# Optimization experiments

Measured on AMD Instinct MI355X. Metric: run time of the kernel, lower is better.

Reference implementation:

```python
import jax, jax.numpy as jnp
import numpy as np

TAU = 0.5  # temperature from init_kwargs


def _semi_loss(h1, h2):
    # GRACE-style InfoNCE: -log( e^{sim(i,i')/tau} / (sum_refl + sum_between - e^{sim(i,i)/tau}) )
    n1 = h1 / jnp.linalg.norm(h1, axis=1, keepdims=True)
    n2 = h2 / jnp.linalg.norm(h2, axis=1, keepdims=True)
    refl = jnp.exp((n1 @ n1.T) / TAU)   # [N, N]
    betw = jnp.exp((n1 @ n2.T) / TAU)   # [N, N]
    denom = refl.sum(axis=1) + betw.sum(axis=1) - jnp.diagonal(refl)
    return -jnp.log(jnp.diagonal(betw) / denom)


def _contrast(h1, h2):
    # forward_v1 with batch_size=0 (batched path is mathematically identical)
    return (0.5 * (_semi_loss(h1, h2) + _semi_loss(h2, h1))).mean()


def _proj(z, Wa, ba, Wb, bb):
    # fc_b(elu(fc_a(z))); torch Linear: y = x @ W.T + b
    return jax.nn.elu(z @ Wa.T + ba) @ Wb.T + bb


def setup_inputs() -> dict:
    key = jax.random.key(0)
    ks = jax.random.split(key, 11)
    N, A, B = 8192, 32, 32
    D = A * B
    s = 1.0 / np.sqrt(D)
    inp = {
        'ta': jax.random.normal(ks[0], (N, A, B), dtype=jnp.float32),
        'tb': jax.random.normal(ks[1], (N, A, B), dtype=jnp.float32),
        'W1': jax.random.uniform(ks[2], (D, D), jnp.float32, -s, s),
        'b1': jax.random.uniform(ks[3], (D,), jnp.float32, -s, s),
        'W2': jax.random.uniform(ks[4], (D, D), jnp.float32, -s, s),
        'b2': jax.random.uniform(ks[5], (D,), jnp.float32, -s, s),
        'W3': jax.random.uniform(ks[6], (D, D), jnp.float32, -s, s),
        'b3': jax.random.uniform(ks[7], (D,), jnp.float32, -s, s),
        'W4': jax.random.uniform(ks[8], (D, D), jnp.float32, -s, s),
        'b4': jax.random.uniform(ks[9], (D,), jnp.float32, -s, s),
        'w_r1': jnp.array([0.5], dtype=jnp.float32),
    }
    return inp


def reference(ta, tb, W1, b1, W2, b2, W3, b3, W4, b4, w_r1):
    N = ta.shape[0]
    # row view: [N, A*B]
    z1 = ta.reshape(N, -1)
    z2 = tb.reshape(N, -1)
    loss_row = _contrast(_proj(z1, W1, b1, W2, b2), _proj(z2, W1, b1, W2, b2))
    # column view: permute(0,2,1) then flatten -> [N, B*A]
    z1c = jnp.transpose(ta, (0, 2, 1)).reshape(N, -1)
    z2c = jnp.transpose(tb, (0, 2, 1)).reshape(N, -1)
    loss_col = _contrast(_proj(z1c, W3, b3, W4, b4), _proj(z2c, W3, b3, W4, b4))
    w_row = jnp.clip(w_r1[0], 0.0, 1.0)
    return w_row * loss_row + (1.0 - w_row) * loss_col
```

## Files before the change

kernel.cpp:

```cpp
#include <hip/hip_runtime.h>
#include <stdint.h>


typedef unsigned short u16;
typedef __attribute__((ext_vector_type(8))) __bf16 bf16x8;
typedef __attribute__((ext_vector_type(4))) float f32x4;

#define NS 8192
#define DD 1024

__device__ __forceinline__ float bf2f(u16 u) {
    union { uint32_t i; float f; } v; v.i = ((uint32_t)u) << 16; return v.f;
}
__device__ __forceinline__ u16 f2bf(float f) {
    union { float f; uint32_t i; } v; v.f = f;
    return (u16)((v.i + 0x7FFFu + ((v.i >> 16) & 1u)) >> 16);
}

__device__ __forceinline__ void gload16(const u16* g, u16* l) {
    __builtin_amdgcn_global_load_lds(
        (__attribute__((address_space(1))) void*)(uintptr_t)(g),
        (__attribute__((address_space(3))) void*)(uintptr_t)(l), 16, 0, 0);
}


__global__ __launch_bounds__(256) void conv_f2bf(const float* __restrict__ src,
                                                 u16* __restrict__ dst) {
    int i = (blockIdx.x * 256 + threadIdx.x) * 4;
    float4 v = *(const float4*)(src + i);
    ushort4 o;
    o.x = f2bf(v.x); o.y = f2bf(v.y); o.z = f2bf(v.z); o.w = f2bf(v.w);
    *(ushort4*)(dst + i) = o;
}

__global__ __launch_bounds__(256) void conv_cat(const float* __restrict__ a,
                                                const float* __restrict__ b,
                                                u16* __restrict__ Z) {
    size_t i = (size_t)(blockIdx.x * 256 + threadIdx.x) * 4;
    const size_t half = (size_t)NS * DD;
    const float* s = (i < half) ? (a + i) : (b + (i - half));
    float4 v = *(const float4*)s;
    ushort4 o;
    o.x = f2bf(v.x); o.y = f2bf(v.y); o.z = f2bf(v.z); o.w = f2bf(v.w);
    *(ushort4*)(Z + i) = o;
}

__global__ __launch_bounds__(256) void conv_col(const float* __restrict__ a,
                                                const float* __restrict__ b,
                                                u16* __restrict__ Z) {
    size_t i = (size_t)(blockIdx.x * 256 + threadIdx.x) * 4;
    const size_t half = (size_t)NS * DD;
    const float* src; size_t o;
    if (i < half) { src = a; o = i; } else { src = b; o = i - half; }
    size_t row = o >> 10;
    int j = (int)(o & 1023);
    int aI = j & 31, bI = j >> 5;
    const float* rp = src + (row << 10);
    ushort4 ov;
    ov.x = f2bf(rp[aI * 32 + bI]);
    ov.y = f2bf(rp[(aI + 1) * 32 + bI]);
    ov.z = f2bf(rp[(aI + 2) * 32 + bI]);
    ov.w = f2bf(rp[(aI + 3) * 32 + bI]);
    *(ushort4*)(Z + i) = ov;
}

template <int MODE>
__global__ __launch_bounds__(256) void gemm_bt(const u16* A, const u16* B,
                                               const float* __restrict__ bias,
                                               u16* __restrict__ out) {
    __shared__ alignas(16) u16 As[128 * 32];
    __shared__ alignas(16) u16 Bs[128 * 32];
    const int tid = threadIdx.x;

    const int tm = blockIdx.y, tn = blockIdx.x;
    const size_t tileM = (size_t)tm * 128;
    const size_t tileN = (size_t)tn * 128;

    const u16* gA0 = A + (tileM + (tid >> 2)) * DD + (tid & 3) * 8;
    const u16* gA1 = gA0 + (size_t)64 * DD;
    const u16* gB0 = B + (tileN + (tid >> 2)) * DD + (tid & 3) * 8;
    const u16* gB1 = gB0 + (size_t)64 * DD;
    u16* lA0 = &As[tid * 8]; u16* lA1 = lA0 + 2048;
    u16* lB0 = &Bs[tid * 8]; u16* lB1 = lB0 + 2048;

    const int lane = tid & 63;
    const int wv = tid >> 6;
    const int wr = (wv >> 1) << 6;
    const int wc = (wv & 1) << 6;
    const int lr = lane & 15;
    const int lh = lane >> 4;

    const u16* aBase = &As[(wr + lr) * 32 + lh * 8];
    const u16* bBase = &Bs[(wc + lr) * 32 + lh * 8];

    f32x4 acc[4][4];
#pragma unroll
    for (int i = 0; i < 4; i++)
#pragma unroll
        for (int j = 0; j < 4; j++) acc[i][j] = (f32x4)0.0f;

    for (int k0 = 0; k0 < DD; k0 += 32) {
        gload16(gA0 + k0, lA0);
        gload16(gA1 + k0, lA1);
        gload16(gB0 + k0, lB0);
        gload16(gB1 + k0, lB1);
        __syncthreads();
        bf16x8 af[4], bfr[4];
#pragma unroll
        for (int rt = 0; rt < 4; rt++) af[rt] = *(const bf16x8*)(aBase + rt * 512);
#pragma unroll
        for (int ct = 0; ct < 4; ct++) bfr[ct] = *(const bf16x8*)(bBase + ct * 512);
#pragma unroll
        for (int rt = 0; rt < 4; rt++)
#pragma unroll
            for (int ct = 0; ct < 4; ct++)
                acc[rt][ct] = __builtin_amdgcn_mfma_f32_16x16x32_bf16(
                    af[rt], bfr[ct], acc[rt][ct], 0, 0, 0);
        __syncthreads();
    }

    float bcol[4];
#pragma unroll
    for (int ct = 0; ct < 4; ct++) bcol[ct] = bias[tileN + wc + ct * 16 + lr];
#pragma unroll
    for (int rt = 0; rt < 4; rt++) {
#pragma unroll
        for (int r = 0; r < 4; r++) {
            size_t row = tileM + wr + rt * 16 + lh * 4 + r;
            u16* orow = out + row * DD + tileN + wc + lr;
#pragma unroll
            for (int ct = 0; ct < 4; ct++) {
                float v = acc[rt][ct][r] + bcol[ct];
                if (MODE == 0) v = v > 0.0f ? v : expm1f(v);
                orow[ct * 16] = f2bf(v);
            }
        }
    }
}

__global__ __launch_bounds__(512) void gram256(const u16* __restrict__ H,
                                               float* __restrict__ S) {
    __shared__ alignas(16) u16 LA[4][256 * 32];
    __shared__ alignas(16) u16 LB[4][256 * 32];
    const int tid = threadIdx.x;

    int x = blockIdx.x, y = blockIdx.y;
    int tm, tn;
    if (y + x < 64) { tm = y;      tn = y + x; }
    else            { tm = 63 - y; tn = x - 1; }

    const size_t rowA = (size_t)tm * 256;
    const size_t rowB = (size_t)tn * 256;

    const int r_lo = tid >> 2;
    const int s_st = tid & 3;
    const int csw  = (s_st ^ (r_lo & 3)) * 8;
    const u16* gA0 = H + (rowA + r_lo) * DD + csw;
    const u16* gA1 = H + (rowA + 128 + r_lo) * DD + csw;
    const u16* gB0 = H + (rowB + r_lo) * DD + csw;
    const u16* gB1 = H + (rowB + 128 + r_lo) * DD + csw;
    const int ldst = tid * 8;

    const int lane = tid & 63;
    const int wv = tid >> 6;
    const int wr = (wv >> 2) * 128;
    const int wc = (wv & 3) * 64;
    const int lr = lane & 15;
    const int lh = lane >> 4;
    const int sw = lh ^ (lr & 3);
    const int aoff = (wr + lr) * 32 + sw * 8;
    const int boff = (wc + lr) * 32 + sw * 8;

    f32x4 acc[8][4];
#pragma unroll
    for (int i = 0; i < 8; ++i)
#pragma unroll
        for (int j = 0; j < 4; ++j) acc[i][j] = (f32x4)0.0f;

#pragma unroll
    for (int t = 0; t < 3; ++t) {
        const int k0 = t * 32;
        gload16(gA0 + k0, &LA[t][0] + ldst);
        gload16(gA1 + k0, &LA[t][4096] + ldst);
        gload16(gB0 + k0, &LB[t][0] + ldst);
        gload16(gB1 + k0, &LB[t][4096] + ldst);
    }
    asm volatile("s_waitcnt vmcnt(8)" ::: "memory");
    __builtin_amdgcn_s_barrier();

    for (int t = 0; t < 32; ++t) {
        const int buf = t & 3;
        const u16* la = &LA[buf][0];
        const u16* lb = &LB[buf][0];
        const int nbuf = (t + 3) & 3;
        const int k0n = (t + 3) * 32;
        bf16x8 aF[4], bF[4];

#pragma unroll
        for (int i = 0; i < 4; ++i) aF[i] = *(const bf16x8*)(la + aoff + i * 512);
#pragma unroll
        for (int i = 0; i < 4; ++i) bF[i] = *(const bf16x8*)(lb + boff + i * 512);
        if (t < 29) {
            gload16(gA0 + k0n, &LA[nbuf][0] + ldst);
            gload16(gA1 + k0n, &LA[nbuf][4096] + ldst);
        }
        asm volatile("" ::: "memory");
        __builtin_amdgcn_s_barrier();
        asm volatile("s_waitcnt lgkmcnt(0)" ::: "memory");
        __builtin_amdgcn_sched_barrier(0);
        __builtin_amdgcn_s_setprio(1);
#pragma unroll
        for (int mi = 0; mi < 4; ++mi)
#pragma unroll
            for (int ni = 0; ni < 4; ++ni)
                acc[mi][ni] = __builtin_amdgcn_mfma_f32_16x16x32_bf16(
                    aF[mi], bF[ni], acc[mi][ni], 0, 0, 0);
        __builtin_amdgcn_s_setprio(0);
        __builtin_amdgcn_s_barrier();

#pragma unroll
        for (int i = 0; i < 4; ++i) aF[i] = *(const bf16x8*)(la + aoff + 2048 + i * 512);
        if (t < 29) {
            gload16(gB0 + k0n, &LB[nbuf][0] + ldst);
            gload16(gB1 + k0n, &LB[nbuf][4096] + ldst);
        }
        if (t < 29)       asm volatile("s_waitcnt vmcnt(8)" ::: "memory");
        else if (t == 29) asm volatile("s_waitcnt vmcnt(4)" ::: "memory");
        else if (t == 30) asm volatile("s_waitcnt vmcnt(0)" ::: "memory");
        __builtin_amdgcn_s_barrier();
        asm volatile("s_waitcnt lgkmcnt(0)" ::: "memory");
        __builtin_amdgcn_sched_barrier(0);
        __builtin_amdgcn_s_setprio(1);
#pragma unroll
        for (int mi = 0; mi < 4; ++mi)
#pragma unroll
            for (int ni = 0; ni < 4; ++ni)
                acc[4 + mi][ni] = __builtin_amdgcn_mfma_f32_16x16x32_bf16(
                    aF[mi], bF[ni], acc[4 + mi][ni], 0, 0, 0);
        __builtin_amdgcn_s_setprio(0);
        __builtin_amdgcn_s_barrier();
    }

    const bool offdiag = (tm != tn);
    float colsum[4] = {0.f, 0.f, 0.f, 0.f};
#pragma unroll
    for (int q = 0; q < 8; ++q) {
#pragma unroll
        for (int r = 0; r < 4; ++r) {
            float rs = 0.0f;
#pragma unroll
            for (int ni = 0; ni < 4; ++ni) {
                float e = __expf(2.0f * acc[q][ni][r]);
                rs += e;
                colsum[ni] += e;
            }
            rs += __shfl_xor(rs, 1);
            rs += __shfl_xor(rs, 2);
            rs += __shfl_xor(rs, 4);
            rs += __shfl_xor(rs, 8);
            if (lr == 0) {
                size_t row = rowA + wr + q * 16 + lh * 4 + r;
                atomicAdd(&S[row], rs);
            }
        }
    }
    if (offdiag) {
#pragma unroll
        for (int ni = 0; ni < 4; ++ni) {
            float cs = colsum[ni];
            cs += __shfl_xor(cs, 16);
            cs += __shfl_xor(cs, 32);
            if (lh == 0) {
                size_t col = rowB + wc + ni * 16 + lr;
                atomicAdd(&S[col], cs);
            }
        }
    }
}

__global__ __launch_bounds__(256) void normalize_kernel(u16* M) {
    __shared__ float red[4];
    const int tid = threadIdx.x;
    u16* row = M + ((size_t)blockIdx.x << 10);
    ushort4 v = ((const ushort4*)row)[tid];
    float x0 = bf2f(v.x), x1 = bf2f(v.y), x2 = bf2f(v.z), x3 = bf2f(v.w);
    float s = x0 * x0 + x1 * x1 + x2 * x2 + x3 * x3;
#pragma unroll
    for (int m = 1; m < 64; m <<= 1) s += __shfl_xor(s, m);
    if ((tid & 63) == 0) red[tid >> 6] = s;
    __syncthreads();
    float inv = rsqrtf(red[0] + red[1] + red[2] + red[3]);
    ushort4 o;
    o.x = f2bf(x0 * inv); o.y = f2bf(x1 * inv);
    o.z = f2bf(x2 * inv); o.w = f2bf(x3 * inv);
    ((ushort4*)row)[tid] = o;
}

__global__ __launch_bounds__(256) void diag_kernel(const u16* M, float* g12) {
    __shared__ float red[4];
    const int tid = threadIdx.x;
    const u16* r1 = M + ((size_t)blockIdx.x << 10);
    const u16* r2 = r1 + ((size_t)NS << 10);
    ushort4 a = ((const ushort4*)r1)[tid];
    ushort4 b = ((const ushort4*)r2)[tid];
    float s = bf2f(a.x) * bf2f(b.x) + bf2f(a.y) * bf2f(b.y) +
              bf2f(a.z) * bf2f(b.z) + bf2f(a.w) * bf2f(b.w);
#pragma unroll
    for (int m = 1; m < 64; m <<= 1) s += __shfl_xor(s, m);
    if ((tid & 63) == 0) red[tid >> 6] = s;
    __syncthreads();
    if (tid == 0) g12[blockIdx.x] = red[0] + red[1] + red[2] + red[3];
}

__global__ __launch_bounds__(256) void final_kernel(const float* Sr, const float* Sc,
                                                    const float* gr, const float* gc,
                                                    const float* w_r1, float* out) {
    __shared__ float red[16];
    const float E2 = 7.389056098930650f;
    float a = 0.f, b = 0.f, c = 0.f, d = 0.f;
    for (int i = threadIdx.x; i < 2 * NS; i += 256) {
        a += logf(Sr[i] - E2);
        b += logf(Sc[i] - E2);
    }
    for (int i = threadIdx.x; i < NS; i += 256) {
        c += gr[i];
        d += gc[i];
    }
#pragma unroll
    for (int m = 1; m < 64; m <<= 1) {
        a += __shfl_xor(a, m); b += __shfl_xor(b, m);
        c += __shfl_xor(c, m); d += __shfl_xor(d, m);
    }
    int w = threadIdx.x >> 6;
    if ((threadIdx.x & 63) == 0) {
        red[w] = a; red[4 + w] = b; red[8 + w] = c; red[12 + w] = d;
    }
    __syncthreads();
    if (threadIdx.x == 0) {
        a = red[0] + red[1] + red[2] + red[3];
        b = red[4] + red[5] + red[6] + red[7];
        c = red[8] + red[9] + red[10] + red[11];
        d = red[12] + red[13] + red[14] + red[15];
        float lr = a / (2.0f * NS) - 2.0f * c / NS;
        float lc = b / (2.0f * NS) - 2.0f * d / NS;
        float w0 = w_r1[0];
        w0 = fminf(fmaxf(w0, 0.0f), 1.0f);
        out[0] = w0 * lr + (1.0f - w0) * lc;
    }
}

extern "C" void kernel_launch(void* const* d_in, const int* in_sizes, int n_in,
                              void* d_out, int out_size, void* d_ws, size_t ws_size,
                              hipStream_t stream) {
    const float* ta = (const float*)d_in[0];
    const float* tb = (const float*)d_in[1];
    const float* W1 = (const float*)d_in[2];
    const float* b1 = (const float*)d_in[3];
    const float* W2 = (const float*)d_in[4];
    const float* b2 = (const float*)d_in[5];
    const float* W3 = (const float*)d_in[6];
    const float* b3 = (const float*)d_in[7];
    const float* W4 = (const float*)d_in[8];
    const float* b4 = (const float*)d_in[9];
    const float* wr = (const float*)d_in[10];
    float* out = (float*)d_out;

    char* p = (char*)d_ws;
    const size_t MAT = (size_t)2 * NS * DD * sizeof(u16);
    u16* Z = (u16*)p;  p += MAT;
    u16* T = (u16*)p;  p += MAT;
    u16* H = (u16*)p;  p += MAT;
    u16* Wb = (u16*)p; p += (size_t)4 * DD * DD * sizeof(u16);
    float* Sr = (float*)p;  p += 2 * NS * sizeof(float);
    float* Sc = (float*)p;  p += 2 * NS * sizeof(float);
    float* gr = (float*)p;  p += NS * sizeof(float);
    float* gc = (float*)p;  p += NS * sizeof(float);

    u16* Wb1 = Wb;
    u16* Wb2 = Wb + (size_t)DD * DD;
    u16* Wb3 = Wb + (size_t)2 * DD * DD;
    u16* Wb4 = Wb + (size_t)3 * DD * DD;

    conv_f2bf<<<1024, 256, 0, stream>>>(W1, Wb1);
    conv_f2bf<<<1024, 256, 0, stream>>>(W2, Wb2);
    conv_f2bf<<<1024, 256, 0, stream>>>(W3, Wb3);
    conv_f2bf<<<1024, 256, 0, stream>>>(W4, Wb4);
    hipMemsetAsync(Sr, 0, 4 * NS * sizeof(float), stream);

    conv_cat<<<16384, 256, 0, stream>>>(ta, tb, Z);
    gemm_bt<0><<<dim3(8, 128), 256, 0, stream>>>(Z, Wb1, b1, T);
    gemm_bt<1><<<dim3(8, 128), 256, 0, stream>>>(T, Wb2, b2, H);
    normalize_kernel<<<16384, 256, 0, stream>>>(H);
    diag_kernel<<<8192, 256, 0, stream>>>(H, gr);
    gram256<<<dim3(65, 32), 512, 0, stream>>>(H, Sr);

    conv_col<<<16384, 256, 0, stream>>>(ta, tb, Z);
    gemm_bt<0><<<dim3(8, 128), 256, 0, stream>>>(Z, Wb3, b3, T);
    gemm_bt<1><<<dim3(8, 128), 256, 0, stream>>>(T, Wb4, b4, H);
    normalize_kernel<<<16384, 256, 0, stream>>>(H);
    diag_kernel<<<8192, 256, 0, stream>>>(H, gc);
    gram256<<<dim3(65, 32), 512, 0, stream>>>(H, Sc);

    final_kernel<<<1, 256, 0, stream>>>(Sr, Sc, gr, gc, wr, out);
}
```

Baseline: 1.273 ms.

## Restructure gram kernel pipeline to one barrier per k-step and fix LDS swizzle

The gram kernel's main loop now does one wait-and-barrier per k-step, loads all eight A fragments and four B fragments at once, issues all four prefetch loads together, then runs 32 MFMAs. Previously each step was split into two half-steps with four barriers. The LDS XOR swizzle in both the gram and projection GEMM kernels now uses bits 2-3 of the row index, aiming to remove bank conflicts on fragment reads. The gram kernel also gets launch_bounds(512,2). Holding more fragments raises register pressure, and a VGPR cap of two blocks per CU could cause spills. Moving the barrier to the loop top also changes the safety of overwriting the ring buffer.

```diff
diff --git a/kernel.cpp b/kernel.cpp
--- a/kernel.cpp
+++ b/kernel.cpp
@@ -76,9 +76,10 @@
     const size_t tileM = (size_t)tm * 128;
     const size_t tileN = (size_t)tn * 128;
 
-    const u16* gA0 = A + (tileM + (tid >> 2)) * DD + (tid & 3) * 8;
+    const int csw = ((tid & 3) ^ ((tid >> 4) & 3)) * 8;
+    const u16* gA0 = A + (tileM + (tid >> 2)) * DD + csw;
     const u16* gA1 = gA0 + (size_t)64 * DD;
-    const u16* gB0 = B + (tileN + (tid >> 2)) * DD + (tid & 3) * 8;
+    const u16* gB0 = B + (tileN + (tid >> 2)) * DD + csw;
     const u16* gB1 = gB0 + (size_t)64 * DD;
     u16* lA0 = &As[tid * 8]; u16* lA1 = lA0 + 2048;
     u16* lB0 = &Bs[tid * 8]; u16* lB1 = lB0 + 2048;
@@ -89,9 +90,10 @@
     const int wc = (wv & 1) << 6;
     const int lr = lane & 15;
     const int lh = lane >> 4;
-
-    const u16* aBase = &As[(wr + lr) * 32 + lh * 8];
-    const u16* bBase = &Bs[(wc + lr) * 32 + lh * 8];
+    const int sw = lh ^ ((lr >> 2) & 3);
+
+    const u16* aBase = &As[(wr + lr) * 32 + sw * 8];
+    const u16* bBase = &Bs[(wc + lr) * 32 + sw * 8];
 
     f32x4 acc[4][4];
 #pragma unroll
@@ -138,8 +140,8 @@
     }
 }
 
-__global__ __launch_bounds__(512) void gram256(const u16* __restrict__ H,
-                                               float* __restrict__ S) {
+__global__ __launch_bounds__(512, 2) void gram256(const u16* __restrict__ H,
+                                                  float* __restrict__ S) {
     __shared__ alignas(16) u16 LA[4][256 * 32];
     __shared__ alignas(16) u16 LB[4][256 * 32];
     const int tid = threadIdx.x;
@@ -153,8 +155,7 @@
     const size_t rowB = (size_t)tn * 256;
 
     const int r_lo = tid >> 2;
-    const int s_st = tid & 3;
-    const int csw  = (s_st ^ (r_lo & 3)) * 8;
+    const int csw  = ((tid & 3) ^ ((r_lo >> 2) & 3)) * 8;
     const u16* gA0 = H + (rowA + r_lo) * DD + csw;
     const u16* gA1 = H + (rowA + 128 + r_lo) * DD + csw;
     const u16* gB0 = H + (rowB + r_lo) * DD + csw;
@@ -167,7 +168,7 @@
     const int wc = (wv & 3) * 64;
     const int lr = lane & 15;
     const int lh = lane >> 4;
-    const int sw = lh ^ (lr & 3);
+    const int sw = lh ^ ((lr >> 2) & 3);
     const int aoff = (wr + lr) * 32 + sw * 8;
     const int boff = (wc + lr) * 32 + sw * 8;
 
@@ -185,60 +186,41 @@
         gload16(gB0 + k0, &LB[t][0] + ldst);
         gload16(gB1 + k0, &LB[t][4096] + ldst);
     }
-    asm volatile("s_waitcnt vmcnt(8)" ::: "memory");
-    __builtin_amdgcn_s_barrier();
 
     for (int t = 0; t < 32; ++t) {
+        if (t < 30)       asm volatile("s_waitcnt vmcnt(8)" ::: "memory");
+        else if (t == 30) asm volatile("s_waitcnt vmcnt(4)" ::: "memory");
+        else              asm volatile("s_waitcnt vmcnt(0)" ::: "memory");
+        __builtin_amdgcn_s_barrier();
+        asm volatile("" ::: "memory");
+
         const int buf = t & 3;
         const u16* la = &LA[buf][0];
         const u16* lb = &LB[buf][0];
-        const int nbuf = (t + 3) & 3;
-        const int k0n = (t + 3) * 32;
-        bf16x8 aF[4], bF[4];
-
-#pragma unroll
-        for (int i = 0; i < 4; ++i) aF[i] = *(const bf16x8*)(la + aoff + i * 512);
+
+        bf16x8 bF[4], aF[8];
 #pragma unroll
         for (int i = 0; i < 4; ++i) bF[i] = *(const bf16x8*)(lb + boff + i * 512);
+#pragma unroll
+        for (int i = 0; i < 8; ++i) aF[i] = *(const bf16x8*)(la + aoff + i * 512);
+
         if (t < 29) {
+            const int nbuf = (t + 3) & 3;
+            const int k0n = (t + 3) * 32;
             gload16(gA0 + k0n, &LA[nbuf][0] + ldst);
             gload16(gA1 + k0n, &LA[nbuf][4096] + ldst);
+            gload16(gB0 + k0n, &LB[nbuf][0] + ldst);
+            gload16(gB1 + k0n, &LB[nbuf][4096] + ldst);
         }
-        asm volatile("" ::: "memory");
-        __builtin_amdgcn_s_barrier();
-        asm volatile("s_waitcnt lgkmcnt(0)" ::: "memory");
-        __builtin_amdgcn_sched_barrier(0);
+
         __builtin_amdgcn_s_setprio(1);
 #pragma unroll
-        for (int mi = 0; mi < 4; ++mi)
+        for (int mi = 0; mi < 8; ++mi)
 #pragma unroll
             for (int ni = 0; ni < 4; ++ni)
                 acc[mi][ni] = __builtin_amdgcn_mfma_f32_16x16x32_bf16(
                     aF[mi], bF[ni], acc[mi][ni], 0, 0, 0);
         __builtin_amdgcn_s_setprio(0);
-        __builtin_amdgcn_s_barrier();
-
-#pragma unroll
-        for (int i = 0; i < 4; ++i) aF[i] = *(const bf16x8*)(la + aoff + 2048 + i * 512);
-        if (t < 29) {
-            gload16(gB0 + k0n, &LB[nbuf][0] + ldst);
-            gload16(gB1 + k0n, &LB[nbuf][4096] + ldst);
-        }
-        if (t < 29)       asm volatile("s_waitcnt vmcnt(8)" ::: "memory");
-        else if (t == 29) asm volatile("s_waitcnt vmcnt(4)" ::: "memory");
-        else if (t == 30) asm volatile("s_waitcnt vmcnt(0)" ::: "memory");
-        __builtin_amdgcn_s_barrier();
-        asm volatile("s_waitcnt lgkmcnt(0)" ::: "memory");
-        __builtin_amdgcn_sched_barrier(0);
-        __builtin_amdgcn_s_setprio(1);
-#pragma unroll
-        for (int mi = 0; mi < 4; ++mi)
-#pragma unroll
-            for (int ni = 0; ni < 4; ++ni)
-                acc[4 + mi][ni] = __builtin_amdgcn_mfma_f32_16x16x32_bf16(
-                    aF[mi], bF[ni], acc[4 + mi][ni], 0, 0, 0);
-        __builtin_amdgcn_s_setprio(0);
-        __builtin_amdgcn_s_barrier();
     }
 
     const bool offdiag = (tm != tn);
```

After: 1.180 ms. -7.3%, faster.
